# Performance work log

Measured on AMD Instinct MI355X. Metric: run time of the kernel, lower is better.

Reference implementation:

```python
import jax, jax.numpy as jnp
import numpy as np

B, T, C = 2, 2048, 1024
NH = 16
HD = C // NH


def setup_inputs() -> dict:
    key = jax.random.key(0)
    k1, k2, k3 = jax.random.split(key, 3)
    x = jax.random.normal(k1, (B, T, C), dtype=jnp.float32)
    w_qkv = jax.random.normal(k2, (C, 3 * C), dtype=jnp.float32) * (C ** -0.5)
    w_proj = jax.random.normal(k3, (C, C), dtype=jnp.float32) * (C ** -0.5)
    return {"x": x, "w_qkv": w_qkv, "w_proj": w_proj}


def reference(x, w_qkv, w_proj):
    Bv, Tv, Cv = x.shape
    qkv = x @ w_qkv  # [B, T, 3C]
    q, k, v = jnp.split(qkv, 3, axis=-1)
    # [B, T, C] -> [B, NH, T, HD]
    q = q.reshape(Bv, Tv, NH, HD).transpose(0, 2, 1, 3)
    k = k.reshape(Bv, Tv, NH, HD).transpose(0, 2, 1, 3)
    v = v.reshape(Bv, Tv, NH, HD).transpose(0, 2, 1, 3)
    att = jnp.einsum("bhqd,bhkd->bhqk", q, k) * (HD ** -0.5)
    causal = jnp.tril(jnp.ones((Tv, Tv), dtype=bool))  # [T, T]
    att = jnp.where(causal[None, None, :, :], att, -jnp.inf)
    att = jax.nn.softmax(att, axis=-1)
    # dropout p=0.0 (eval) -> identity
    y = jnp.einsum("bhqk,bhkd->bhqd", att, v)  # [B, NH, T, HD]
    y = y.transpose(0, 2, 1, 3).reshape(Bv, Tv, Cv)
    return y @ w_proj
```

## Files before the change

kernel.cpp:

```cpp
#include <hip/hip_runtime.h>
#include <hip/hip_bf16.h>

#define B_ 2
#define T_ 2048
#define C_ 1024
#define NH_ 16
#define HD_ 64

using bf16 = __hip_bfloat16;
typedef __attribute__((ext_vector_type(8))) short bf16x8;
typedef __attribute__((ext_vector_type(4))) float f32x4;

__device__ __forceinline__ float bf2f(unsigned short u) {
    union { unsigned int i; float f; } v;
    v.i = ((unsigned int)u) << 16;
    return v.f;
}
__device__ __forceinline__ unsigned short f2bf(float f) {
    union { float f; unsigned int u; } v;
    v.f = f;
    unsigned int r = v.u + 0x7fffu + ((v.u >> 16) & 1u);
    return (unsigned short)(r >> 16);
}
__device__ __forceinline__ unsigned int cvt_pk_bf16(float lo, float hi) {
    unsigned int r;
    asm("v_cvt_pk_bf16_f32 %0, %1, %2" : "=v"(r) : "v"(lo), "v"(hi));
    return r;
}
__device__ __forceinline__ void gld_lds16(const void* g, void* l) {
    __builtin_amdgcn_global_load_lds(
        (__attribute__((address_space(1))) void*)g,
        (__attribute__((address_space(3))) void*)l, 16, 0, 0);
}

__global__ __launch_bounds__(256) void cast_bf16(
    const float* __restrict__ X, unsigned short* __restrict__ Xb, int n) {
    int i = (blockIdx.x * 256 + threadIdx.x) * 8;
    if (i >= n) return;
    float4 f0 = *reinterpret_cast<const float4*>(&X[i]);
    float4 f1 = *reinterpret_cast<const float4*>(&X[i + 4]);
    union { unsigned short s[8]; uint4 v; } o;
    o.s[0] = f2bf(f0.x); o.s[1] = f2bf(f0.y); o.s[2] = f2bf(f0.z); o.s[3] = f2bf(f0.w);
    o.s[4] = f2bf(f1.x); o.s[5] = f2bf(f1.y); o.s[6] = f2bf(f1.z); o.s[7] = f2bf(f1.w);
    *reinterpret_cast<uint4*>(&Xb[i]) = o.v;
}

__global__ __launch_bounds__(256) void transpose_cast(
    const float* __restrict__ W, unsigned short* __restrict__ Wt, int NN, int KK) {
    __shared__ short S[64][72];
    const int t = threadIdx.x;
    const int k0 = blockIdx.y * 64, n0 = blockIdx.x * 64;
    const int lr = t >> 2, lc = (t & 3) * 16;
    const float* src = &W[(size_t)(k0 + lr) * NN + n0 + lc];
    #pragma unroll
    for (int j4 = 0; j4 < 4; ++j4) {
        float4 f = *reinterpret_cast<const float4*>(src + j4 * 4);
        S[lc + j4 * 4 + 0][lr] = (short)f2bf(f.x);
        S[lc + j4 * 4 + 1][lr] = (short)f2bf(f.y);
        S[lc + j4 * 4 + 2][lr] = (short)f2bf(f.z);
        S[lc + j4 * 4 + 3][lr] = (short)f2bf(f.w);
    }
    __syncthreads();
    union { unsigned short s[16]; uint4 v[2]; } o;
    #pragma unroll
    for (int j = 0; j < 16; ++j) o.s[j] = (unsigned short)S[lr][lc + j];
    unsigned short* dst = &Wt[(size_t)(n0 + lr) * KK + k0 + lc];
    *reinterpret_cast<uint4*>(dst)     = o.v[0];
    *reinterpret_cast<uint4*>(dst + 8) = o.v[1];
}

__global__ __launch_bounds__(256) void transpose_v(
    const unsigned short* __restrict__ V, unsigned short* __restrict__ Vt) {
    __shared__ short S[64][72];
    const int t  = threadIdx.x;
    const int bh = blockIdx.y;
    const int t0 = blockIdx.x * 64;
    const int lr = t >> 2, lc = (t & 3) * 16;
    const unsigned short* src = V + ((size_t)bh * T_ + t0 + lr) * HD_ + lc;
    union { uint4 v[2]; unsigned short s[16]; } u;
    u.v[0] = *reinterpret_cast<const uint4*>(src);
    u.v[1] = *reinterpret_cast<const uint4*>(src + 8);
    #pragma unroll
    for (int j = 0; j < 16; ++j) S[lc + j][lr] = (short)u.s[j];
    __syncthreads();
    union { unsigned short s[16]; uint4 v[2]; } o;
    #pragma unroll
    for (int j = 0; j < 16; ++j) o.s[j] = (unsigned short)S[lr][lc + j];
    unsigned short* dst = Vt + ((size_t)bh * HD_ + lr) * T_ + t0 + lc;
    *reinterpret_cast<uint4*>(dst)     = o.v[0];
    *reinterpret_cast<uint4*>(dst + 8) = o.v[1];
}

__global__ __launch_bounds__(256) void qkv_gemm_mfma(
    const unsigned short* __restrict__ A, const unsigned short* __restrict__ Bt,
    unsigned short* __restrict__ Qb, unsigned short* __restrict__ Kb,
    unsigned short* __restrict__ Vb) {
    __shared__ short As[128 * 32];
    __shared__ short Bs[128 * 32];
    const int t = threadIdx.x;
    const int wid = t >> 6, lane = t & 63;
    const int wm = wid >> 1, wn = wid & 1;
    const int c = lane & 15, g = lane >> 4;
    const int dd = blockIdx.x;
    const int w  = (dd & 7) * 96 + (dd >> 3);
    const int m0 = (w / 24) * 128, n0 = (w % 24) * 128;
    const int K = C_;
    const int srow = t >> 2, skk = (t & 3) * 8;

    f32x4 acc[4][4];
    #pragma unroll
    for (int i = 0; i < 4; ++i)
        #pragma unroll
        for (int j = 0; j < 4; ++j) acc[i][j] = (f32x4){0.f, 0.f, 0.f, 0.f};

    for (int k0 = 0; k0 < K; k0 += 32) {
        __syncthreads();
        gld_lds16(&A[(size_t)(m0 + srow) * K + k0 + skk],       As + t * 8);
        gld_lds16(&A[(size_t)(m0 + 64 + srow) * K + k0 + skk],  As + 2048 + t * 8);
        gld_lds16(&Bt[(size_t)(n0 + srow) * K + k0 + skk],      Bs + t * 8);
        gld_lds16(&Bt[(size_t)(n0 + 64 + srow) * K + k0 + skk], Bs + 2048 + t * 8);
        __syncthreads();
        bf16x8 af[4], bfv[4];
        #pragma unroll
        for (int mi = 0; mi < 4; ++mi)
            af[mi] = *reinterpret_cast<const bf16x8*>(&As[(wm * 64 + mi * 16 + c) * 32 + g * 8]);
        #pragma unroll
        for (int ni = 0; ni < 4; ++ni)
            bfv[ni] = *reinterpret_cast<const bf16x8*>(&Bs[(wn * 64 + ni * 16 + c) * 32 + g * 8]);
        #pragma unroll
        for (int mi = 0; mi < 4; ++mi)
            #pragma unroll
            for (int ni = 0; ni < 4; ++ni)
                acc[mi][ni] = __builtin_amdgcn_mfma_f32_16x16x32_bf16(af[mi], bfv[ni], acc[mi][ni], 0, 0, 0);
    }

    const int nbase = n0 + wn * 64;
    const int which = nbase >> 10;
    const int h     = (nbase >> 6) & (NH_ - 1);
    const float scale = (which == 0) ? 0.125f * 1.44269504f : 1.0f;
    unsigned short* dst = (which == 0) ? Qb : ((which == 1) ? Kb : Vb);
    #pragma unroll
    for (int mi = 0; mi < 4; ++mi)
        #pragma unroll
        for (int r = 0; r < 4; ++r) {
            const int m = m0 + wm * 64 + mi * 16 + 4 * g + r;
            const int bb = m >> 11, tq = m & (T_ - 1);
            unsigned short* p = dst + ((size_t)((bb << 4) | h) * T_ + tq) * HD_;
            #pragma unroll
            for (int ni = 0; ni < 4; ++ni)
                p[ni * 16 + c] = f2bf(acc[mi][ni][r] * scale);
        }
}

__global__ __launch_bounds__(256) void proj_gemm_mfma(
    const unsigned short* __restrict__ A, const unsigned short* __restrict__ Bt,
    float* __restrict__ Out) {
    __shared__ short As[64 * 32];
    __shared__ short Bs[128 * 32];
    const int t = threadIdx.x;
    const int wid = t >> 6, lane = t & 63;
    const int wm = wid >> 1, wn = wid & 1;
    const int c = lane & 15, g = lane >> 4;
    const int m0 = blockIdx.y * 64, n0 = blockIdx.x * 128;
    const int K = C_;
    const int srow = t >> 2, skk = (t & 3) * 8;

    f32x4 acc[2][4];
    #pragma unroll
    for (int i = 0; i < 2; ++i)
        #pragma unroll
        for (int j = 0; j < 4; ++j) acc[i][j] = (f32x4){0.f, 0.f, 0.f, 0.f};

    for (int k0 = 0; k0 < K; k0 += 32) {
        __syncthreads();
        gld_lds16(&A[(size_t)(m0 + srow) * K + k0 + skk],       As + t * 8);
        gld_lds16(&Bt[(size_t)(n0 + srow) * K + k0 + skk],      Bs + t * 8);
        gld_lds16(&Bt[(size_t)(n0 + 64 + srow) * K + k0 + skk], Bs + 2048 + t * 8);
        __syncthreads();
        bf16x8 af[2], bfv[4];
        #pragma unroll
        for (int mi = 0; mi < 2; ++mi)
            af[mi] = *reinterpret_cast<const bf16x8*>(&As[(wm * 32 + mi * 16 + c) * 32 + g * 8]);
        #pragma unroll
        for (int ni = 0; ni < 4; ++ni)
            bfv[ni] = *reinterpret_cast<const bf16x8*>(&Bs[(wn * 64 + ni * 16 + c) * 32 + g * 8]);
        #pragma unroll
        for (int mi = 0; mi < 2; ++mi)
            #pragma unroll
            for (int ni = 0; ni < 4; ++ni)
                acc[mi][ni] = __builtin_amdgcn_mfma_f32_16x16x32_bf16(af[mi], bfv[ni], acc[mi][ni], 0, 0, 0);
    }

    #pragma unroll
    for (int mi = 0; mi < 2; ++mi)
        #pragma unroll
        for (int r = 0; r < 4; ++r) {
            const int m = m0 + wm * 32 + mi * 16 + 4 * g + r;
            float* p = Out + (size_t)m * C_ + n0 + wn * 64;
            #pragma unroll
            for (int ni = 0; ni < 4; ++ni)
                p[ni * 16 + c] = acc[mi][ni][r];
        }
}

__global__ __launch_bounds__(512) void attn_mfma(
    const unsigned short* __restrict__ Qb, const unsigned short* __restrict__ Kb,
    const unsigned short* __restrict__ Vt_g, unsigned short* __restrict__ Yu) {
    __shared__ short Ks[2][64][72];
    __shared__ short Vt[2][64][72];
    __shared__ short Ps[8][16][72];

    const int t    = threadIdx.x;
    const int wid  = t >> 6;
    const int lane = t & 63;
    const int c    = lane & 15;
    const int g    = lane >> 4;

    const int d   = blockIdx.x;
    const int xcd = d & 7;
    const int tt  = d >> 3;
    const int up  = tt & 15;
    const int k2  = tt >> 4;
    const int bh  = (k2 << 3) | xcd;
    const int u   = (k2 & 2) ? (15 - up) : up;
    const int qtB = 2 * u + 1;
    const int myqt = (wid < 4) ? (2 * u) : qtB;

    const int bb = bh >> 4, h = bh & (NH_ - 1);
    const int qw0 = (wid & 3) * 16;
    const int q0  = myqt * 64;

    const unsigned short* Qh  = Qb   + (size_t)bh * T_ * HD_;
    const unsigned short* Kh  = Kb   + (size_t)bh * T_ * HD_;
    const unsigned short* VTh = Vt_g + (size_t)bh * HD_ * T_;

    const int srow = t >> 3, scol = (t & 7) * 8;

    bf16x8 qf0, qf1;
    {
        const unsigned short* qs = Qh + (size_t)(q0 + qw0 + c) * HD_ + g * 8;
        qf0 = *reinterpret_cast<const bf16x8*>(qs);
        qf1 = *reinterpret_cast<const bf16x8*>(qs + 32);
    }

    float m_run = -1e30f, l_run = 0.f;
    f32x4 yacc[4];
    #pragma unroll
    for (int nt = 0; nt < 4; ++nt) yacc[nt] = (f32x4){0.f, 0.f, 0.f, 0.f};

    uint4 kv, vv;
    {
        kv = *reinterpret_cast<const uint4*>(&Kh[(size_t)srow * HD_ + scol]);
        vv = *reinterpret_cast<const uint4*>(&VTh[(size_t)srow * T_ + scol]);
    }

    #pragma unroll 1
    for (int kt = 0; kt <= qtB; ++kt) {
        const int cur = kt & 1;
        *reinterpret_cast<uint4*>(&Ks[cur][srow][scol]) = kv;
        *reinterpret_cast<uint4*>(&Vt[cur][srow][scol]) = vv;
        __syncthreads();

        if (kt < qtB) {
            const int j1 = (kt + 1) * 64;
            kv = *reinterpret_cast<const uint4*>(&Kh[(size_t)(j1 + srow) * HD_ + scol]);
            vv = *reinterpret_cast<const uint4*>(&VTh[(size_t)srow * T_ + j1 + scol]);
        }

        if (kt <= myqt) {
            f32x4 sacc[4];
            #pragma unroll
            for (int nt = 0; nt < 4; ++nt) sacc[nt] = (f32x4){0.f, 0.f, 0.f, 0.f};
            __builtin_amdgcn_s_setprio(1);
            #pragma unroll
            for (int kk = 0; kk < 2; ++kk) {
                const bf16x8 qf = kk ? qf1 : qf0;
                #pragma unroll
                for (int nt = 0; nt < 4; ++nt) {
                    bf16x8 kf = *reinterpret_cast<const bf16x8*>(&Ks[cur][nt * 16 + c][kk * 32 + g * 8]);
                    sacc[nt] = __builtin_amdgcn_mfma_f32_16x16x32_bf16(kf, qf, sacc[nt], 0, 0, 0);
                }
            }
            __builtin_amdgcn_s_setprio(0);

            float p[4][4];
            const bool diag = (kt == myqt);
            #pragma unroll
            for (int nt = 0; nt < 4; ++nt)
                #pragma unroll
                for (int r = 0; r < 4; ++r) {
                    float s = sacc[nt][r];
                    if (diag && (nt * 16 + 4 * g + r > qw0 + c)) s = -1e30f;
                    p[nt][r] = s;
                }
            float t0 = fmaxf(fmaxf(p[0][0], p[0][1]), fmaxf(p[0][2], p[0][3]));
            float t1 = fmaxf(fmaxf(p[1][0], p[1][1]), fmaxf(p[1][2], p[1][3]));
            float t2 = fmaxf(fmaxf(p[2][0], p[2][1]), fmaxf(p[2][2], p[2][3]));
            float t3 = fmaxf(fmaxf(p[3][0], p[3][1]), fmaxf(p[3][2], p[3][3]));
            float tmax = fmaxf(fmaxf(t0, t1), fmaxf(t2, t3));
            tmax = fmaxf(tmax, __shfl_xor(tmax, 16, 64));
            tmax = fmaxf(tmax, __shfl_xor(tmax, 32, 64));

            if (!__all(tmax <= m_run + 8.0f)) {
                const float mnew = fmaxf(m_run, tmax);
                const float sc   = exp2f(m_run - mnew);
                m_run = mnew;
                l_run *= sc;
                const int sci = __float_as_int(sc);
                #pragma unroll
                for (int r = 0; r < 4; ++r) {
                    float scr = __int_as_float(__builtin_amdgcn_ds_bpermute((4 * g + r) * 4, sci));
                    #pragma unroll
                    for (int nt = 0; nt < 4; ++nt) yacc[nt][r] *= scr;
                }
            }

            float lsum = 0.f;
            #pragma unroll
            for (int nt = 0; nt < 4; ++nt)
                #pragma unroll
                for (int r = 0; r < 4; ++r) {
                    p[nt][r] = exp2f(p[nt][r] - m_run);
                    lsum += p[nt][r];
                }
            l_run += lsum;

            #pragma unroll
            for (int nt = 0; nt < 4; ++nt) {
                uint2 pw;
                pw.x = cvt_pk_bf16(p[nt][0], p[nt][1]);
                pw.y = cvt_pk_bf16(p[nt][2], p[nt][3]);
                *reinterpret_cast<uint2*>(&Ps[wid][c][nt * 16 + 4 * g]) = pw;
            }

            __builtin_amdgcn_s_setprio(1);
            #pragma unroll
            for (int kk = 0; kk < 2; ++kk) {
                bf16x8 pa = *reinterpret_cast<const bf16x8*>(&Ps[wid][c][kk * 32 + g * 8]);
                #pragma unroll
                for (int nt = 0; nt < 4; ++nt) {
                    bf16x8 vb = *reinterpret_cast<const bf16x8*>(&Vt[cur][nt * 16 + c][kk * 32 + g * 8]);
                    yacc[nt] = __builtin_amdgcn_mfma_f32_16x16x32_bf16(pa, vb, yacc[nt], 0, 0, 0);
                }
            }
            __builtin_amdgcn_s_setprio(0);
        }
    }

    float lf = l_run;
    lf += __shfl_xor(lf, 16, 64);
    lf += __shfl_xor(lf, 32, 64);
    const float inv = 1.0f / lf;
    const int ii = __float_as_int(inv);
    float invr[4];
    #pragma unroll
    for (int r = 0; r < 4; ++r)
        invr[r] = __int_as_float(__builtin_amdgcn_ds_bpermute((4 * g + r) * 4, ii));
    #pragma unroll
    for (int r = 0; r < 4; ++r) {
        const size_t row = (size_t)(bb * T_ + q0 + qw0 + 4 * g + r);
        #pragma unroll
        for (int nt = 0; nt < 4; ++nt) {
            const int col = h * HD_ + 16 * nt + c;
            Yu[row * C_ + col] = f2bf(yacc[nt][r] * invr[r]);
        }
    }
}

extern "C" void kernel_launch(void* const* d_in, const int* in_sizes, int n_in,
                              void* d_out, int out_size, void* d_ws, size_t ws_size,
                              hipStream_t stream) {
    const float* x      = (const float*)d_in[0];
    const float* w_qkv  = (const float*)d_in[1];
    const float* w_proj = (const float*)d_in[2];
    float* out = (float*)d_out;

    const size_t HELEMS = (size_t)B_ * NH_ * T_ * HD_;
    unsigned short* Qb   = (unsigned short*)d_ws;
    unsigned short* Kb   = Qb + HELEMS;
    unsigned short* Vraw = Kb + HELEMS;
    unsigned short* Yb   = Vraw;
    unsigned short* Xb   = Vraw + HELEMS;
    unsigned short* Vt   = Xb;
    unsigned short* Wqt  = Xb + HELEMS;
    unsigned short* Wpt  = Wqt;

    const int NX = B_ * T_ * C_;
    cast_bf16<<<NX / (256 * 8), 256, 0, stream>>>(x, Xb, NX);
    transpose_cast<<<dim3(48, 16), 256, 0, stream>>>(w_qkv, Wqt, 3 * C_, C_);
    qkv_gemm_mfma<<<768, 256, 0, stream>>>(Xb, Wqt, Qb, Kb, Vraw);
    transpose_v<<<dim3(32, 32), 256, 0, stream>>>(Vraw, Vt);
    transpose_cast<<<dim3(16, 16), 256, 0, stream>>>(w_proj, Wpt, C_, C_);
    attn_mfma<<<512, 512, 0, stream>>>(Qb, Kb, Vt, Yb);
    proj_gemm_mfma<<<dim3(8, 64), 256, 0, stream>>>(Yb, Wpt, out);
}
```

Before: 121.5 us.

## Software-pipeline QK^T of next tile with softmax and PV of previous tile

Restructures the attention inner loop so each iteration computes the QK^T scores for the current key tile and then runs softmax and the PV product for the previous tile. K/V shared buffers grow from double to triple buffering so the previous tile's V stays resident. This lets score MFMAs overlap with exp and max work on the prior tile, at the cost of more registers, extra LDS and a tail step after the loop. The max-reduction tree is also reshaped slightly.

```diff
diff --git a/kernel.cpp b/kernel.cpp
--- a/kernel.cpp
+++ b/kernel.cpp
@@ -206,8 +206,8 @@
 __global__ __launch_bounds__(512) void attn_mfma(
     const unsigned short* __restrict__ Qb, const unsigned short* __restrict__ Kb,
     const unsigned short* __restrict__ Vt_g, unsigned short* __restrict__ Yu) {
-    __shared__ short Ks[2][64][72];
-    __shared__ short Vt[2][64][72];
+    __shared__ short Ks[3][64][72];
+    __shared__ short Vt[3][64][72];
     __shared__ short Ps[8][16][72];
 
     const int t    = threadIdx.x;
@@ -248,6 +248,76 @@
     #pragma unroll
     for (int nt = 0; nt < 4; ++nt) yacc[nt] = (f32x4){0.f, 0.f, 0.f, 0.f};
 
+    f32x4 sprev[4];
+    bool have_prev = false;
+    bool prev_diag = false;
+
+    auto process = [&](int pb, bool diag) {
+        float p[4][4];
+        #pragma unroll
+        for (int nt = 0; nt < 4; ++nt)
+            #pragma unroll
+            for (int r = 0; r < 4; ++r) {
+                float s = sprev[nt][r];
+                if (diag && (nt * 16 + 4 * g + r > qw0 + c)) s = -1e30f;
+                p[nt][r] = s;
+            }
+        float a0 = fmaxf(fmaxf(p[0][0], p[0][1]), p[0][2]);
+        float a1 = fmaxf(fmaxf(p[0][3], p[1][0]), p[1][1]);
+        float a2 = fmaxf(fmaxf(p[1][2], p[1][3]), p[2][0]);
+        float a3 = fmaxf(fmaxf(p[2][1], p[2][2]), p[2][3]);
+        float a4 = fmaxf(fmaxf(p[3][0], p[3][1]), p[3][2]);
+        float b0 = fmaxf(fmaxf(a0, a1), a2);
+        float b1 = fmaxf(fmaxf(a3, a4), p[3][3]);
+        float tmax = fmaxf(b0, b1);
+        tmax = fmaxf(tmax, __shfl_xor(tmax, 16, 64));
+        tmax = fmaxf(tmax, __shfl_xor(tmax, 32, 64));
+
+        if (!__all(tmax <= m_run + 8.0f)) {
+            const float mnew = fmaxf(m_run, tmax);
+            const float sc   = exp2f(m_run - mnew);
+            m_run = mnew;
+            l_run *= sc;
+            const int sci = __float_as_int(sc);
+            #pragma unroll
+            for (int r = 0; r < 4; ++r) {
+                float scr = __int_as_float(__builtin_amdgcn_ds_bpermute((4 * g + r) * 4, sci));
+                #pragma unroll
+                for (int nt = 0; nt < 4; ++nt) yacc[nt][r] *= scr;
+            }
+        }
+
+        float lsum = 0.f;
+        #pragma unroll
+        for (int nt = 0; nt < 4; ++nt)
+            #pragma unroll
+            for (int r = 0; r < 4; ++r) {
+                p[nt][r] = exp2f(p[nt][r] - m_run);
+                lsum += p[nt][r];
+            }
+        l_run += lsum;
+
+        #pragma unroll
+        for (int nt = 0; nt < 4; ++nt) {
+            uint2 pw;
+            pw.x = cvt_pk_bf16(p[nt][0], p[nt][1]);
+            pw.y = cvt_pk_bf16(p[nt][2], p[nt][3]);
+            *reinterpret_cast<uint2*>(&Ps[wid][c][nt * 16 + 4 * g]) = pw;
+        }
+
+        __builtin_amdgcn_s_setprio(1);
+        #pragma unroll
+        for (int kk = 0; kk < 2; ++kk) {
+            bf16x8 pa = *reinterpret_cast<const bf16x8*>(&Ps[wid][c][kk * 32 + g * 8]);
+            #pragma unroll
+            for (int nt = 0; nt < 4; ++nt) {
+                bf16x8 vb = *reinterpret_cast<const bf16x8*>(&Vt[pb][nt * 16 + c][kk * 32 + g * 8]);
+                yacc[nt] = __builtin_amdgcn_mfma_f32_16x16x32_bf16(pa, vb, yacc[nt], 0, 0, 0);
+            }
+        }
+        __builtin_amdgcn_s_setprio(0);
+    };
+
     uint4 kv, vv;
     {
         kv = *reinterpret_cast<const uint4*>(&Kh[(size_t)srow * HD_ + scol]);
@@ -256,7 +326,7 @@
 
     #pragma unroll 1
     for (int kt = 0; kt <= qtB; ++kt) {
-        const int cur = kt & 1;
+        const int cur = kt % 3;
         *reinterpret_cast<uint4*>(&Ks[cur][srow][scol]) = kv;
         *reinterpret_cast<uint4*>(&Vt[cur][srow][scol]) = vv;
         __syncthreads();
@@ -267,10 +337,11 @@
             vv = *reinterpret_cast<const uint4*>(&VTh[(size_t)srow * T_ + j1 + scol]);
         }
 
-        if (kt <= myqt) {
-            f32x4 sacc[4];
-            #pragma unroll
-            for (int nt = 0; nt < 4; ++nt) sacc[nt] = (f32x4){0.f, 0.f, 0.f, 0.f};
+        const bool active = (kt <= myqt);
+        f32x4 snew[4];
+        if (active) {
+            #pragma unroll
+            for (int nt = 0; nt < 4; ++nt) snew[nt] = (f32x4){0.f, 0.f, 0.f, 0.f};
             __builtin_amdgcn_s_setprio(1);
             #pragma unroll
             for (int kk = 0; kk < 2; ++kk) {
@@ -278,74 +349,24 @@
                 #pragma unroll
                 for (int nt = 0; nt < 4; ++nt) {
                     bf16x8 kf = *reinterpret_cast<const bf16x8*>(&Ks[cur][nt * 16 + c][kk * 32 + g * 8]);
-                    sacc[nt] = __builtin_amdgcn_mfma_f32_16x16x32_bf16(kf, qf, sacc[nt], 0, 0, 0);
+                    snew[nt] = __builtin_amdgcn_mfma_f32_16x16x32_bf16(kf, qf, snew[nt], 0, 0, 0);
                 }
             }
             __builtin_amdgcn_s_setprio(0);
-
-            float p[4][4];
-            const bool diag = (kt == myqt);
-            #pragma unroll
-            for (int nt = 0; nt < 4; ++nt)
-                #pragma unroll
-                for (int r = 0; r < 4; ++r) {
-                    float s = sacc[nt][r];
-                    if (diag && (nt * 16 + 4 * g + r > qw0 + c)) s = -1e30f;
-                    p[nt][r] = s;
-                }
-            float t0 = fmaxf(fmaxf(p[0][0], p[0][1]), fmaxf(p[0][2], p[0][3]));
-            float t1 = fmaxf(fmaxf(p[1][0], p[1][1]), fmaxf(p[1][2], p[1][3]));
-            float t2 = fmaxf(fmaxf(p[2][0], p[2][1]), fmaxf(p[2][2], p[2][3]));
-            float t3 = fmaxf(fmaxf(p[3][0], p[3][1]), fmaxf(p[3][2], p[3][3]));
-            float tmax = fmaxf(fmaxf(t0, t1), fmaxf(t2, t3));
-            tmax = fmaxf(tmax, __shfl_xor(tmax, 16, 64));
-            tmax = fmaxf(tmax, __shfl_xor(tmax, 32, 64));
-
-            if (!__all(tmax <= m_run + 8.0f)) {
-                const float mnew = fmaxf(m_run, tmax);
-                const float sc   = exp2f(m_run - mnew);
-                m_run = mnew;
-                l_run *= sc;
-                const int sci = __float_as_int(sc);
-                #pragma unroll
-                for (int r = 0; r < 4; ++r) {
-                    float scr = __int_as_float(__builtin_amdgcn_ds_bpermute((4 * g + r) * 4, sci));
-                    #pragma unroll
-                    for (int nt = 0; nt < 4; ++nt) yacc[nt][r] *= scr;
-                }
-            }
-
-            float lsum = 0.f;
-            #pragma unroll
-            for (int nt = 0; nt < 4; ++nt)
-                #pragma unroll
-                for (int r = 0; r < 4; ++r) {
-                    p[nt][r] = exp2f(p[nt][r] - m_run);
-                    lsum += p[nt][r];
-                }
-            l_run += lsum;
-
-            #pragma unroll
-            for (int nt = 0; nt < 4; ++nt) {
-                uint2 pw;
-                pw.x = cvt_pk_bf16(p[nt][0], p[nt][1]);
-                pw.y = cvt_pk_bf16(p[nt][2], p[nt][3]);
-                *reinterpret_cast<uint2*>(&Ps[wid][c][nt * 16 + 4 * g]) = pw;
-            }
-
-            __builtin_amdgcn_s_setprio(1);
-            #pragma unroll
-            for (int kk = 0; kk < 2; ++kk) {
-                bf16x8 pa = *reinterpret_cast<const bf16x8*>(&Ps[wid][c][kk * 32 + g * 8]);
-                #pragma unroll
-                for (int nt = 0; nt < 4; ++nt) {
-                    bf16x8 vb = *reinterpret_cast<const bf16x8*>(&Vt[cur][nt * 16 + c][kk * 32 + g * 8]);
-                    yacc[nt] = __builtin_amdgcn_mfma_f32_16x16x32_bf16(pa, vb, yacc[nt], 0, 0, 0);
-                }
-            }
-            __builtin_amdgcn_s_setprio(0);
-        }
-    }
+        }
+
+        if (have_prev) {
+            process((kt + 2) % 3, prev_diag);
+            have_prev = false;
+        }
+        if (active) {
+            #pragma unroll
+            for (int nt = 0; nt < 4; ++nt) sprev[nt] = snew[nt];
+            prev_diag = (kt == myqt);
+            have_prev = true;
+        }
+    }
+    if (have_prev) process(qtB % 3, prev_diag);
 
     float lf = l_run;
     lf += __shfl_xor(lf, 16, 64);
```

Result: slower. 124.4 us (+2.4%).
